# Kernel optimization log

Hardware: AMD Instinct MI355X
Metric: run time of the kernel (lower is better)

## Reference

```python
import jax, jax.numpy as jnp
from jax import lax
import numpy as np

NEG = -1e30


def setup_inputs() -> dict:
    key = jax.random.key(0)
    k0, k1, k2, k3 = jax.random.split(key, 4)
    B, txt_T, mel_T, n_mel = 32, 256, 2048, 80
    mu_logvar = jax.random.normal(k0, (B, txt_T, 2 * n_mel), jnp.float32)
    melspec = jax.random.normal(k1, (B, n_mel, mel_T), jnp.float32)
    text_lengths = jax.random.randint(k2, (B,), txt_T // 2, txt_T + 1)
    mel_lengths = jax.random.randint(k3, (B,), mel_T // 2, mel_T + 1)
    return dict(mu_logvar=mu_logvar, melspec=melspec,
                text_lengths=text_lengths, mel_lengths=mel_lengths)


def _log_prob_matrix(mu_logvar, melspec):
    # Gaussian log-prob (mean over mel channels), expanded into GEMM form:
    # -0.5/n_mel * sum_c [ (x_c - mu_c)^2 * exp(-logvar_c) + logvar_c ]
    n_mel = melspec.shape[1]
    mu = mu_logvar[..., :n_mel]           # [B, txt_T, C]
    logvar = mu_logvar[..., n_mel:]       # [B, txt_T, C]
    x = jnp.swapaxes(melspec, 1, 2)       # [B, mel_T, C]
    inv_var = jnp.exp(-logvar)
    t1 = jnp.einsum('btc,bjc->bjt', x * x, inv_var)        # sum x^2/var
    t2 = jnp.einsum('btc,bjc->bjt', x, mu * inv_var)       # sum x*mu/var
    t3 = jnp.sum(mu * mu * inv_var, axis=-1)               # [B, txt_T]
    t4 = jnp.sum(logvar, axis=-1)                          # [B, txt_T]
    return -0.5 * (t1 - 2.0 * t2 + (t3 + t4)[:, :, None]) / n_mel  # [B, txt_T, mel_T]


def _mdn_loss(mu_logvar, melspec, text_lengths, mel_lengths):
    log_prob = _log_prob_matrix(mu_logvar, melspec)   # [B, txt_T, mel_T]
    B, txt_T, mel_T = log_prob.shape
    col0 = jnp.full((B, txt_T), NEG, log_prob.dtype).at[:, 0].set(log_prob[:, 0, 0])

    def step(col, lp_t):
        shifted = jnp.concatenate([jnp.full((B, 1), NEG, col.dtype), col[:, :-1]], axis=1)
        new = jnp.logaddexp(col, shifted) + lp_t
        return new, new

    lp_rest = jnp.moveaxis(log_prob[:, :, 1:], 2, 0)  # [mel_T-1, B, txt_T]
    _, cols = lax.scan(step, col0, lp_rest)
    log_alpha = jnp.concatenate([col0[None], cols], axis=0)  # [mel_T, B, txt_T]

    b = jnp.arange(B)
    alpha_last = log_alpha[mel_lengths - 1, b, text_lengths - 1]
    alpha_last = alpha_last / mel_lengths.astype(log_prob.dtype)
    return -alpha_last.mean(), log_prob


def reference(mu_logvar, melspec, text_lengths, mel_lengths):
    mdn_loss, log_prob_matrix = _mdn_loss(mu_logvar, melspec, text_lengths, mel_lengths)
    return mdn_loss, log_prob_matrix
```

## Files before the change

### kernel.cpp

```cpp
#include <hip/hip_runtime.h>
#include <cstddef>
#include <cstdint>

#define NEGV -1e30f

constexpr int B_    = 32;
constexpr int TXT   = 256;
constexpr int MEL   = 2048;
constexpr int NMEL  = 80;

#define INV_LN2 1.4426950408889634f
#define LN2     0.6931471805599453f

__global__ __launch_bounds__(256) void precompute_kernel(
    const float* __restrict__ mu_logvar,
    float* __restrict__ IV, float* __restrict__ M2, float* __restrict__ S)
{
    const int b = blockIdx.x;
    const int j = threadIdx.x;
    const float* row = mu_logvar + (size_t)(b * TXT + j) * (2 * NMEL);
    float s = 0.f;
    for (int c = 0; c < NMEL; ++c) {
        float mu = row[c];
        float lv = row[NMEL + c];
        float iv = expf(-lv);
        IV[(b * NMEL + c) * TXT + j] = iv;
        M2[(b * NMEL + c) * TXT + j] = 2.0f * mu * iv;
        s += mu * mu * iv + lv;
    }
    S[b * TXT + j] = s;
}

__global__ __launch_bounds__(256) void logprob_kernel(
    const float* __restrict__ mel,
    const float* __restrict__ IV, const float* __restrict__ M2,
    const float* __restrict__ S,
    float* __restrict__ out1,
    float* __restrict__ lpT,
    int write_lpT)
{
    const int tt0 = blockIdx.x * 128;
    const int j0  = blockIdx.y * 64;
    const int b   = blockIdx.z;
    const int tx  = threadIdx.x & 15;
    const int ty  = threadIdx.x >> 4;

    __shared__ union SM {
        struct { float IV[NMEL][64]; float M2[NMEL][64]; } stage;
        float V[64][132];
    } sm;

    for (int idx = threadIdx.x; idx < NMEL * 64; idx += 256) {
        int c  = idx >> 6;
        int jj = idx & 63;
        sm.stage.IV[c][jj] = IV[(b * NMEL + c) * TXT + j0 + jj];
        sm.stage.M2[c][jj] = M2[(b * NMEL + c) * TXT + j0 + jj];
    }
    __syncthreads();

    float acc[4][8];
#pragma unroll
    for (int a = 0; a < 4; ++a)
#pragma unroll
        for (int d = 0; d < 8; ++d) acc[a][d] = 0.f;

    const float* melb = mel + (size_t)b * NMEL * MEL + tt0 + tx;

#pragma unroll 2
    for (int c = 0; c < NMEL; ++c) {
        float x[8];
#pragma unroll
        for (int d = 0; d < 8; ++d) x[d] = melb[(size_t)c * MEL + 16 * d];
        float4 iv = *(const float4*)&sm.stage.IV[c][ty * 4];
        float4 m2 = *(const float4*)&sm.stage.M2[c][ty * 4];
        float ivr[4] = {iv.x, iv.y, iv.z, iv.w};
        float m2r[4] = {m2.x, m2.y, m2.z, m2.w};
#pragma unroll
        for (int a = 0; a < 4; ++a) {
#pragma unroll
            for (int d = 0; d < 8; ++d) {
                float tmp = fmaf(ivr[a], x[d], -m2r[a]);
                acc[a][d] = fmaf(tmp, x[d], acc[a][d]);
            }
        }
    }

    const float c0 = -0.5f / (float)NMEL;
    float4 sj = *(const float4*)&S[b * TXT + j0 + ty * 4];
    float sjr[4] = {sj.x, sj.y, sj.z, sj.w};

    __syncthreads();
#pragma unroll
    for (int a = 0; a < 4; ++a) {
        const int jl = ty * 4 + a;
#pragma unroll
        for (int d = 0; d < 8; ++d) {
            sm.V[jl][tx + 16 * d] = c0 * (acc[a][d] + sjr[a]);
        }
    }
    __syncthreads();

    const int tid = threadIdx.x;

    {
        const int t4 = (tid & 31) * 4;
        const int jb = tid >> 5;
#pragma unroll
        for (int k = 0; k < 8; ++k) {
            const int jl = jb + 8 * k;
            float4 v = *(const float4*)&sm.V[jl][t4];
            *(float4*)&out1[(size_t)(b * TXT + j0 + jl) * MEL + tt0 + t4] = v;
        }
    }

    if (write_lpT) {
        const int j4 = (tid & 15) * 4;
        const int tb = tid >> 4;
#pragma unroll
        for (int k = 0; k < 8; ++k) {
            const int tl = tb + 16 * k;
            float4 v;
            v.x = sm.V[j4 + 0][tl] * INV_LN2;
            v.y = sm.V[j4 + 1][tl] * INV_LN2;
            v.z = sm.V[j4 + 2][tl] * INV_LN2;
            v.w = sm.V[j4 + 3][tl] * INV_LN2;
            *(float4*)&lpT[((size_t)b * MEL + tt0 + tl) * TXT + j0 + j4] = v;
        }
    }
}

typedef float f32x4 __attribute__((ext_vector_type(4)));

__device__ __forceinline__ float wave_ror1(float x) {
    int xi = __float_as_int(x);
    int r  = __builtin_amdgcn_update_dpp(xi, xi, 0x13C , 0xF, 0xF, false);
    return __int_as_float(r);
}

__device__ __forceinline__ float exp2_nat(float x) {
#if __has_builtin(__builtin_amdgcn_exp2f)
    return __builtin_amdgcn_exp2f(x);
#else
    float r; asm("v_exp_f32 %0, %1" : "=v"(r) : "v"(x)); return r;
#endif
}

__device__ __forceinline__ float log2_nat(float x) {
#if __has_builtin(__builtin_amdgcn_logf)
    return __builtin_amdgcn_logf(x);
#else
    float r; asm("v_log_f32 %0, %1" : "=v"(r) : "v"(x)); return r;
#endif
}

__device__ __forceinline__ float lse2b_lp(float a, float b, float lp) {
    float mx   = fmaxf(a, b);
    float d    = -fabsf(a - b);
    float base = mx + lp;
    return base + log2_nat(1.0f + exp2_nat(d));
}

__global__ __launch_bounds__(64, 1) void dp_kernel(
    const float* __restrict__ lpT,
    const int* __restrict__ tlen, const int* __restrict__ mlen,
    float* __restrict__ alpha)
{
    const int b = blockIdx.x;
    const int l = threadIdx.x;

    const int tl   = tlen[b];
    const int ml   = mlen[b];
    const int tmax = ml - 1;
    const int jt   = tl - 1;
    const float out_scale = LN2 / (float)ml;

    const float* sbase = lpT + (size_t)b * MEL * TXT;
    const bool z = (l == 0);

    __shared__ float ring[32][256];

    f32x4 ld0 = *(const f32x4*)(sbase + l * 4);
    float c0 = z ? ld0[0] : NEGV;
    float c1 = NEGV, c2 = NEGV, c3 = NEGV;

    if (tmax <= 0) {
        const int lf = jt >> 2, ef = jt & 3;
        float v = (ef == 0) ? c0 : NEGV;
        if (l == lf) alpha[b] = v * out_scale;
        return;
    }

    __builtin_amdgcn_sched_barrier(0);

#define ISSUE(R)                                                              \
    __builtin_amdgcn_global_load_lds(                                         \
        (const __attribute__((address_space(1))) void*)(sbase + (size_t)(R) * TXT + l * 4), \
        (__attribute__((address_space(3))) void*)&ring[(R) & 31][0],          \
        16, 0, 0)

#pragma unroll
    for (int r = 1; r <= 16; ++r) ISSUE(r);

    asm volatile("s_waitcnt vmcnt(12)" ::: "memory");
    __builtin_amdgcn_sched_barrier(0);
    f32x4 cur0 = *(const f32x4*)&ring[1][l * 4];
    f32x4 cur1 = *(const f32x4*)&ring[2][l * 4];
    f32x4 cur2 = *(const f32x4*)&ring[3][l * 4];
    f32x4 cur3 = *(const f32x4*)&ring[4][l * 4];

#define DP_CORE(LP)                                            \
    {                                                          \
        float sw = wave_ror1(c3);                              \
        sw = z ? NEGV : sw;                                    \
        float n0 = lse2b_lp(c0, sw, (LP)[0]);                  \
        float n1 = lse2b_lp(c1, c0, (LP)[1]);                  \
        float n2 = lse2b_lp(c2, c1, (LP)[2]);                  \
        float n3 = lse2b_lp(c3, c2, (LP)[3]);                  \
        c0 = n0; c1 = n1; c2 = n2; c3 = n3;                    \
    }

    int t = 1;
    for (; t + 7 <= tmax; t += 4) {
        ISSUE(t + 16); ISSUE(t + 17); ISSUE(t + 18); ISSUE(t + 19);
        asm volatile("s_waitcnt vmcnt(12)" ::: "memory");
        __builtin_amdgcn_sched_barrier(0);
        f32x4 n0v = *(const f32x4*)&ring[(t + 4) & 31][l * 4];
        f32x4 n1v = *(const f32x4*)&ring[(t + 5) & 31][l * 4];
        f32x4 n2v = *(const f32x4*)&ring[(t + 6) & 31][l * 4];
        f32x4 n3v = *(const f32x4*)&ring[(t + 7) & 31][l * 4];
        DP_CORE(cur0); DP_CORE(cur1); DP_CORE(cur2); DP_CORE(cur3);
        cur0 = n0v; cur1 = n1v; cur2 = n2v; cur3 = n3v;
    }

    asm volatile("s_waitcnt vmcnt(0)" ::: "memory");
    __builtin_amdgcn_sched_barrier(0);

    DP_CORE(cur0);
    if (t + 1 <= tmax) DP_CORE(cur1);
    if (t + 2 <= tmax) DP_CORE(cur2);
    if (t + 3 <= tmax) DP_CORE(cur3);
#pragma unroll
    for (int k = 4; k <= 6; ++k) {
        if (t + k <= tmax) {
            f32x4 rr = *(const f32x4*)&ring[(t + k) & 31][l * 4];
            DP_CORE(rr);
        }
    }

#undef DP_CORE
#undef ISSUE

    const int lf = jt >> 2;
    const int ef = jt & 3;
    float v = (ef == 0) ? c0 : (ef == 1) ? c1 : (ef == 2) ? c2 : c3;
    if (l == lf) alpha[b] = v * out_scale;
}

__global__ __launch_bounds__(256) void dp_kernel_fallback(
    const float* __restrict__ lp,
    const int* __restrict__ tlen, const int* __restrict__ mlen,
    float* __restrict__ alpha)
{
    const int b    = blockIdx.x;
    const int j    = threadIdx.x;
    const int lane = j & 63;
    const int w    = j >> 6;

    const int tl   = tlen[b];
    const int ml   = mlen[b];
    const int tmax = ml - 1;
    const int jt   = tl - 1;
    const float inv_ml = 1.0f / (float)ml;

    __shared__ float bnd[2][4];
    if (threadIdx.x < 8) bnd[threadIdx.x >> 2][threadIdx.x & 3] = NEGV;
    __syncthreads();

    float cur = (j == 0) ? lp[(size_t)(b * TXT) * MEL] : NEGV;
    if (tmax == 0) {
        if (j == jt) alpha[b] = cur * inv_ml;
        return;
    }
    int p = 0;
    for (int t = 1; t <= tmax; ++t) {
        float lpc = lp[((size_t)(b * TXT + j)) * MEL + t];
        float sh = __shfl_up(cur, 1);
        if (lane == 0) sh = (w > 0) ? bnd[p][w - 1] : NEGV;
        float mx = fmaxf(cur, sh);
        float dd = fminf(cur, sh) - mx;
        float nv = mx + __logf(1.0f + __expf(dd)) + lpc;
        if (lane == 63) bnd[p ^ 1][w] = nv;
        if (t == tmax && j == jt) alpha[b] = nv * inv_ml;
        cur = nv;
        __syncthreads();
        p ^= 1;
    }
}

__global__ void reduce_kernel(const float* __restrict__ alpha, float* __restrict__ out)
{
    const int tid = threadIdx.x;
    float v = (tid < B_) ? alpha[tid] : 0.f;
#pragma unroll
    for (int m = 16; m >= 1; m >>= 1) v += __shfl_xor(v, m);
    if (tid == 0) out[0] = -v / (float)B_;
}

extern "C" void kernel_launch(void* const* d_in, const int* in_sizes, int n_in,
                              void* d_out, int out_size, void* d_ws, size_t ws_size,
                              hipStream_t stream)
{
    const float* mu_logvar = (const float*)d_in[0];
    const float* melspec   = (const float*)d_in[1];
    const int*   tlen      = (const int*)d_in[2];
    const int*   mlen      = (const int*)d_in[3];
    float* out = (float*)d_out;
    float* ws  = (float*)d_ws;

    const size_t IV_OFF    = 0;
    const size_t M2_OFF    = 655360;
    const size_t S_OFF     = 1310720;
    const size_t ALPHA_OFF = 1318912;
    const size_t LPT_OFF   = 1318944;
    const size_t LPT_ELEMS = (size_t)B_ * MEL * TXT;
    const size_t LPT_PAD   = (size_t)16 * TXT;

    float* IV    = ws + IV_OFF;
    float* M2    = ws + M2_OFF;
    float* S     = ws + S_OFF;
    float* alpha = ws + ALPHA_OFF;
    float* lpT   = ws + LPT_OFF;

    const bool use_lpT = ws_size >= (LPT_OFF + LPT_ELEMS + LPT_PAD) * sizeof(float);

    precompute_kernel<<<dim3(B_), dim3(256), 0, stream>>>(mu_logvar, IV, M2, S);

    logprob_kernel<<<dim3(MEL / 128, TXT / 64, B_), dim3(256), 0, stream>>>(
        melspec, IV, M2, S, out + 1, lpT, use_lpT ? 1 : 0);

    if (use_lpT) {
        dp_kernel<<<dim3(B_), dim3(64), 0, stream>>>(lpT, tlen, mlen, alpha);
    } else {
        dp_kernel_fallback<<<dim3(B_), dim3(256), 0, stream>>>(out + 1, tlen, mlen, alpha);
    }

    reduce_kernel<<<dim3(1), dim3(64), 0, stream>>>(alpha, out);
}
```

Baseline: 357.6 us.

## Run alignment DP in scaled linear space instead of log-space

The GEMM epilogue now stores exp2 of the log-probabilities, so the DP works on plain probabilities. It keeps a per-lane integer exponent that is aligned across lanes through DPP, and renormalises every four steps. This swaps the exp/log pair in each log-add-exp on the serial recurrence for ldexp, add and multiply ops. The cost is per-step exponent bookkeeping, a periodic renormalisation, and some risk of underflow or precision loss. Any fallback path that reads lpT as log values would also become inconsistent.

```diff
diff --git a/kernel.cpp b/kernel.cpp
--- a/kernel.cpp
+++ b/kernel.cpp
@@ -11,6 +11,40 @@
 
 #define INV_LN2 1.4426950408889634f
 #define LN2     0.6931471805599453f
+#define M_DEAD  (-(1 << 30))
+
+typedef float f32x4 __attribute__((ext_vector_type(4)));
+
+__device__ __forceinline__ float wave_ror1_f(float x) {
+    int xi = __float_as_int(x);
+    int r  = __builtin_amdgcn_update_dpp(xi, xi, 0x13C , 0xF, 0xF, false);
+    return __int_as_float(r);
+}
+__device__ __forceinline__ int wave_ror1_i(int x) {
+    return __builtin_amdgcn_update_dpp(x, x, 0x13C , 0xF, 0xF, false);
+}
+
+__device__ __forceinline__ float exp2_nat(float x) {
+#if __has_builtin(__builtin_amdgcn_exp2f)
+    return __builtin_amdgcn_exp2f(x);
+#else
+    float r; asm("v_exp_f32 %0, %1" : "=v"(r) : "v"(x)); return r;
+#endif
+}
+__device__ __forceinline__ float log2_nat(float x) {
+#if __has_builtin(__builtin_amdgcn_logf)
+    return __builtin_amdgcn_logf(x);
+#else
+    float r; asm("v_log_f32 %0, %1" : "=v"(r) : "v"(x)); return r;
+#endif
+}
+__device__ __forceinline__ float ldexp_nat(float x, int n) {
+#if __has_builtin(__builtin_amdgcn_ldexpf)
+    return __builtin_amdgcn_ldexpf(x, n);
+#else
+    float r; asm("v_ldexp_f32 %0, %1, %2" : "=v"(r) : "v"(x), "v"(n)); return r;
+#endif
+}
 
 __global__ __launch_bounds__(256) void precompute_kernel(
     const float* __restrict__ mu_logvar,
@@ -120,44 +154,13 @@
         for (int k = 0; k < 8; ++k) {
             const int tl = tb + 16 * k;
             float4 v;
-            v.x = sm.V[j4 + 0][tl] * INV_LN2;
-            v.y = sm.V[j4 + 1][tl] * INV_LN2;
-            v.z = sm.V[j4 + 2][tl] * INV_LN2;
-            v.w = sm.V[j4 + 3][tl] * INV_LN2;
+            v.x = exp2_nat(sm.V[j4 + 0][tl] * INV_LN2);
+            v.y = exp2_nat(sm.V[j4 + 1][tl] * INV_LN2);
+            v.z = exp2_nat(sm.V[j4 + 2][tl] * INV_LN2);
+            v.w = exp2_nat(sm.V[j4 + 3][tl] * INV_LN2);
             *(float4*)&lpT[((size_t)b * MEL + tt0 + tl) * TXT + j0 + j4] = v;
         }
     }
-}
-
-typedef float f32x4 __attribute__((ext_vector_type(4)));
-
-__device__ __forceinline__ float wave_ror1(float x) {
-    int xi = __float_as_int(x);
-    int r  = __builtin_amdgcn_update_dpp(xi, xi, 0x13C , 0xF, 0xF, false);
-    return __int_as_float(r);
-}
-
-__device__ __forceinline__ float exp2_nat(float x) {
-#if __has_builtin(__builtin_amdgcn_exp2f)
-    return __builtin_amdgcn_exp2f(x);
-#else
-    float r; asm("v_exp_f32 %0, %1" : "=v"(r) : "v"(x)); return r;
-#endif
-}
-
-__device__ __forceinline__ float log2_nat(float x) {
-#if __has_builtin(__builtin_amdgcn_logf)
-    return __builtin_amdgcn_logf(x);
-#else
-    float r; asm("v_log_f32 %0, %1" : "=v"(r) : "v"(x)); return r;
-#endif
-}
-
-__device__ __forceinline__ float lse2b_lp(float a, float b, float lp) {
-    float mx   = fmaxf(a, b);
-    float d    = -fabsf(a - b);
-    float base = mx + lp;
-    return base + log2_nat(1.0f + exp2_nat(d));
 }
 
 __global__ __launch_bounds__(64, 1) void dp_kernel(
@@ -180,13 +183,17 @@
     __shared__ float ring[32][256];
 
     f32x4 ld0 = *(const f32x4*)(sbase + l * 4);
-    float c0 = z ? ld0[0] : NEGV;
-    float c1 = NEGV, c2 = NEGV, c3 = NEGV;
+    int   ex0 = (int)(__float_as_uint(ld0[0]) >> 23) - 126;
+    float q0n = ldexp_nat(ld0[0], -ex0);
+    float q0 = z ? q0n : 0.f;
+    float q1 = 0.f, q2 = 0.f, q3 = 0.f;
+    int   M  = z ? ex0 : M_DEAD;
 
     if (tmax <= 0) {
-        const int lf = jt >> 2, ef = jt & 3;
-        float v = (ef == 0) ? c0 : NEGV;
-        if (l == lf) alpha[b] = v * out_scale;
+        if (l == (jt >> 2)) {
+            float vv = (jt == 0) ? log2_nat(ld0[0]) : NEGV;
+            alpha[b] = vv * out_scale;
+        }
         return;
     }
 
@@ -208,15 +215,36 @@
     f32x4 cur2 = *(const f32x4*)&ring[3][l * 4];
     f32x4 cur3 = *(const f32x4*)&ring[4][l * 4];
 
-#define DP_CORE(LP)                                            \
+#define DP_CORE(P)                                             \
     {                                                          \
-        float sw = wave_ror1(c3);                              \
-        sw = z ? NEGV : sw;                                    \
-        float n0 = lse2b_lp(c0, sw, (LP)[0]);                  \
-        float n1 = lse2b_lp(c1, c0, (LP)[1]);                  \
-        float n2 = lse2b_lp(c2, c1, (LP)[2]);                  \
-        float n3 = lse2b_lp(c3, c2, (LP)[3]);                  \
-        c0 = n0; c1 = n1; c2 = n2; c3 = n3;                    \
+        float qb = wave_ror1_f(q3);                            \
+        int   Mb = wave_ror1_i(M);                             \
+        qb = z ? 0.f : qb;                                     \
+        int Mc  = (M > Mb) ? M : Mb;                           \
+        int dql = M - Mc;                                      \
+        int dqb = Mb - Mc;                                     \
+        float qbs = ldexp_nat(qb, dqb);                        \
+        float a0 = ldexp_nat(q0, dql);                         \
+        float a1 = ldexp_nat(q1, dql);                         \
+        float a2 = ldexp_nat(q2, dql);                         \
+        float a3 = ldexp_nat(q3, dql);                         \
+        q0 = (a0 + qbs) * (P)[0];                              \
+        q1 = (a1 + a0)  * (P)[1];                              \
+        q2 = (a2 + a1)  * (P)[2];                              \
+        q3 = (a3 + a2)  * (P)[3];                              \
+        M = Mc;                                                \
+    }
+
+#define RENORM()                                               \
+    {                                                          \
+        float mloc = fmaxf(fmaxf(q0, q1), fmaxf(q2, q3));      \
+        int ex = (int)(__float_as_uint(mloc) >> 23) - 126;     \
+        int nex = -ex;                                         \
+        q0 = ldexp_nat(q0, nex);                               \
+        q1 = ldexp_nat(q1, nex);                               \
+        q2 = ldexp_nat(q2, nex);                               \
+        q3 = ldexp_nat(q3, nex);                               \
+        M = (mloc > 0.f) ? (M + ex) : M_DEAD;                  \
     }
 
     int t = 1;
@@ -229,6 +257,7 @@
         f32x4 n2v = *(const f32x4*)&ring[(t + 6) & 31][l * 4];
         f32x4 n3v = *(const f32x4*)&ring[(t + 7) & 31][l * 4];
         DP_CORE(cur0); DP_CORE(cur1); DP_CORE(cur2); DP_CORE(cur3);
+        RENORM();
         cur0 = n0v; cur1 = n1v; cur2 = n2v; cur3 = n3v;
     }
 
@@ -239,6 +268,7 @@
     if (t + 1 <= tmax) DP_CORE(cur1);
     if (t + 2 <= tmax) DP_CORE(cur2);
     if (t + 3 <= tmax) DP_CORE(cur3);
+    RENORM();
 #pragma unroll
     for (int k = 4; k <= 6; ++k) {
         if (t + k <= tmax) {
@@ -247,13 +277,14 @@
         }
     }
 
+#undef RENORM
 #undef DP_CORE
 #undef ISSUE
 
     const int lf = jt >> 2;
     const int ef = jt & 3;
-    float v = (ef == 0) ? c0 : (ef == 1) ? c1 : (ef == 2) ? c2 : c3;
-    if (l == lf) alpha[b] = v * out_scale;
+    float v = (ef == 0) ? q0 : (ef == 1) ? q1 : (ef == 2) ? q2 : q3;
+    if (l == lf) alpha[b] = (log2_nat(v) + (float)M) * out_scale;
 }
 
 __global__ __launch_bounds__(256) void dp_kernel_fallback(
```

Measured after the change: 315.2 us. -11.9%, faster.
